# Performance work log

Hardware: AMD Instinct MI355X
Metric: run time of the kernel (lower is better)

The kernel has to match this reference:

```python
import jax, jax.numpy as jnp
import numpy as np

T = 4194304  # sequence length (2**22)

def setup_inputs() -> dict:
    key = jax.random.key(0)
    k = jax.random.split(key, 7)
    return {
        "x_0": jax.random.normal(k[0], (1, 2), dtype=jnp.float32),
        "u": jax.random.normal(k[1], (2, T), dtype=jnp.float32),
        "timedelta": jax.random.uniform(k[2], (T,), dtype=jnp.float32),
        # scale W_A down so the linear recurrence x_t = A x_{t-1} + ... is stable over 4M steps
        "W_A": 0.3 * jax.random.normal(k[3], (2, 2), dtype=jnp.float32),
        "b_A": 0.1 * jax.random.normal(k[4], (2,), dtype=jnp.float32),
        "W_B": jax.random.normal(k[5], (2, 2), dtype=jnp.float32),
        "b_B": 0.1 * jax.random.normal(k[6], (2,), dtype=jnp.float32),
    }

def reference(x_0, u, timedelta, W_A, b_A, W_B, b_B):
    # forward_PINN: linear state recurrence x_t = A x_{t-1} + B u_t (+biases),
    # output_t = physics_prediction(x_{t-1}, u_t, dt_t) - x_t
    x0 = x_0[0]          # [2] state (x, y)
    u_seq = u.T          # [T, 2] controls (speed, heading)

    def step(x_prev, inp):
        u_t, dt = inp                                  # [2], scalar
        x_t = W_A @ x_prev + b_A + W_B @ u_t + b_B     # [2]
        c = u_t[0] * dt
        pinn = x_prev + jnp.stack([c * jnp.cos(u_t[1]), c * jnp.sin(u_t[1])])
        return x_t, pinn - x_t

    _, x_out = jax.lax.scan(step, x0, (u_seq, timedelta))  # [T, 2]
    return x_out
```

## Files before the change

kernel.cpp:

```cpp
#include <hip/hip_runtime.h>

#define T_TOTAL 4194304
#define S 16
#define NTHREADS 256
#define BLOCK_T (NTHREADS * S)
#define HALO_SEG 4
#define NSEG (NTHREADS + HALO_SEG)

struct M22 { float m00, m01, m10, m11; };
__device__ __forceinline__ M22 mmul(const M22& X, const M22& Y) {
    M22 r;
    r.m00 = fmaf(X.m00, Y.m00, X.m01 * Y.m10);
    r.m01 = fmaf(X.m00, Y.m01, X.m01 * Y.m11);
    r.m10 = fmaf(X.m10, Y.m00, X.m11 * Y.m10);
    r.m11 = fmaf(X.m10, Y.m01, X.m11 * Y.m11);
    return r;
}

struct alignas(16) F16 { float f[16]; };
__device__ __forceinline__ void load16(F16& d, const float* __restrict__ p) {
    const float4* q = (const float4*)p;
    float4 a0 = q[0], a1 = q[1], a2 = q[2], a3 = q[3];
    *(float4*)&d.f[0]  = a0;
    *(float4*)&d.f[4]  = a1;
    *(float4*)&d.f[8]  = a2;
    *(float4*)&d.f[12] = a3;
}

__global__ __launch_bounds__(NTHREADS, 4)
void pinn_rnn_kernel(const float* __restrict__ x0p,
                     const float* __restrict__ u,
                     const float* __restrict__ td,
                     const float* __restrict__ WA,
                     const float* __restrict__ bA,
                     const float* __restrict__ WB,
                     const float* __restrict__ bB,
                     float* __restrict__ out)
{
    __shared__ float2 lc[NSEG];
    __shared__ float2 lout[BLOCK_T];

    const int tid = threadIdx.x;
    const int B0  = blockIdx.x * BLOCK_T;

    const float a00 = WA[0], a01 = WA[1], a10 = WA[2], a11 = WA[3];
    const float w00 = WB[0], w01 = WB[1], w10 = WB[2], w11 = WB[3];
    const float bc0 = bA[0] + bB[0];
    const float bc1 = bA[1] + bB[1];

    const float* u0 = u;
    const float* u1 = u + T_TOTAL;

    const int t0 = B0 + tid * S;
    F16 U0, U1, DT;
    load16(U0, u0 + t0);
    load16(U1, u1 + t0);
    load16(DT, td + t0);

    M22 A   = { a00, a01, a10, a11 };
    M22 A2  = mmul(A,  A );
    M22 A4  = mmul(A2, A2);
    M22 A8  = mmul(A4, A4);
    M22 M   = mmul(A8, A8);
    M22 Mp2 = mmul(M,  M );
    M22 Mp3 = mmul(Mp2, M);

    {
        float x0v = 0.f, x1v = 0.f;
        #pragma unroll
        for (int j = 0; j < S; ++j) {
            float v0 = fmaf(w00, U0.f[j], fmaf(w01, U1.f[j], bc0));
            float v1 = fmaf(w10, U0.f[j], fmaf(w11, U1.f[j], bc1));
            float n0 = fmaf(a00, x0v, fmaf(a01, x1v, v0));
            float n1 = fmaf(a10, x0v, fmaf(a11, x1v, v1));
            x0v = n0; x1v = n1;
        }
        lc[tid + HALO_SEG] = make_float2(x0v, x1v);
    }
    if (tid < HALO_SEG) {
        float2 ch = make_float2(0.f, 0.f);
        if (blockIdx.x != 0) {
            const int th = B0 - HALO_SEG * S + tid * S;
            F16 H0, H1;
            load16(H0, u0 + th);
            load16(H1, u1 + th);
            float x0v = 0.f, x1v = 0.f;
            #pragma unroll
            for (int j = 0; j < S; ++j) {
                float v0 = fmaf(w00, H0.f[j], fmaf(w01, H1.f[j], bc0));
                float v1 = fmaf(w10, H0.f[j], fmaf(w11, H1.f[j], bc1));
                float n0 = fmaf(a00, x0v, fmaf(a01, x1v, v0));
                float n1 = fmaf(a10, x0v, fmaf(a11, x1v, v1));
                x0v = n0; x1v = n1;
            }
            ch = make_float2(x0v, x1v);
        }
        lc[tid] = ch;
    }
    __syncthreads();

    float2 c1 = lc[tid + 3], c2 = lc[tid + 2], c3 = lc[tid + 1], c4 = lc[tid];
    float xi0 = c1.x
              + fmaf(M.m00,   c2.x, M.m01   * c2.y)
              + fmaf(Mp2.m00, c3.x, Mp2.m01 * c3.y)
              + fmaf(Mp3.m00, c4.x, Mp3.m01 * c4.y);
    float xi1 = c1.y
              + fmaf(M.m10,   c2.x, M.m11   * c2.y)
              + fmaf(Mp2.m10, c3.x, Mp2.m11 * c3.y)
              + fmaf(Mp3.m10, c4.x, Mp3.m11 * c4.y);

    if (blockIdx.x == 0 && tid < HALO_SEG) {
        float X0 = x0p[0], X1 = x0p[1];
        M22 P;
        if      (tid == 0) P = { 1.f, 0.f, 0.f, 1.f };
        else if (tid == 1) P = M;
        else if (tid == 2) P = Mp2;
        else               P = Mp3;
        xi0 += fmaf(P.m00, X0, P.m01 * X1);
        xi1 += fmaf(P.m10, X0, P.m11 * X1);
    }

    {
        const int xm = tid & 14;
        float2* lrow = lout + tid * S;
        float x0v = xi0, x1v = xi1;
        #pragma unroll
        for (int j = 0; j < S; ++j) {
            float v0 = fmaf(w00, U0.f[j], fmaf(w01, U1.f[j], bc0));
            float v1 = fmaf(w10, U0.f[j], fmaf(w11, U1.f[j], bc1));
            float n0 = fmaf(a00, x0v, fmaf(a01, x1v, v0));
            float n1 = fmaf(a10, x0v, fmaf(a11, x1v, v1));
            float cc = U0.f[j] * DT.f[j];
            float sn, cs;
            __sincosf(U1.f[j], &sn, &cs);
            lrow[j ^ xm] = make_float2(fmaf(cc, cs, x0v) - n0,
                                       fmaf(cc, sn, x1v) - n1);
            x0v = n0; x1v = n1;
        }
    }
    __syncthreads();

    const float4* lo4 = (const float4*)lout;
    float4* og = (float4*)out + (B0 >> 1);
    #pragma unroll
    for (int m = 0; m < 8; ++m) {
        int f    = m * NTHREADS + tid;
        int i0   = f << 1;
        int slot = i0 ^ ((i0 >> 4) & 14);
        og[f] = lo4[slot >> 1];
    }
}

extern "C" void kernel_launch(void* const* d_in, const int* in_sizes, int n_in,
                              void* d_out, int out_size, void* d_ws, size_t ws_size,
                              hipStream_t stream) {
    const float* x0p = (const float*)d_in[0];
    const float* u   = (const float*)d_in[1];
    const float* td  = (const float*)d_in[2];
    const float* WA  = (const float*)d_in[3];
    const float* bA  = (const float*)d_in[4];
    const float* WB  = (const float*)d_in[5];
    const float* bB  = (const float*)d_in[6];
    float* outp = (float*)d_out;

    dim3 grid(T_TOTAL / BLOCK_T);
    dim3 block(NTHREADS);
    pinn_rnn_kernel<<<grid, block, 0, stream>>>(x0p, u, td, WA, bA, WB, bB, outp);
}
```

Before: 106.6 us.

## Stage input loads through swizzled shared memory for coalesced global reads

Replaces the per-thread strided 64-byte vector loads of u and timedelta with fully coalesced block-wide float4 loads into a swizzled LDS buffer, which each thread then reads back as its contiguous 16-element chunk. The same LDS buffer is reused for u, then timedelta, then the output staging, so the shared-memory footprint stays the same. The aim is better global-load coalescing. In exchange it adds several barriers and LDS round trips, and the timedelta load is deferred until after the chunk-state scan.

```diff
diff --git a/kernel.cpp b/kernel.cpp
--- a/kernel.cpp
+++ b/kernel.cpp
@@ -18,13 +18,9 @@
 }
 
 struct alignas(16) F16 { float f[16]; };
-__device__ __forceinline__ void load16(F16& d, const float* __restrict__ p) {
-    const float4* q = (const float4*)p;
-    float4 a0 = q[0], a1 = q[1], a2 = q[2], a3 = q[3];
-    *(float4*)&d.f[0]  = a0;
-    *(float4*)&d.f[4]  = a1;
-    *(float4*)&d.f[8]  = a2;
-    *(float4*)&d.f[12] = a3;
+
+__device__ __forceinline__ int swz(int t, int o) {
+    return (t << 2) | (o ^ ((t >> 1) & 3));
 }
 
 __global__ __launch_bounds__(NTHREADS, 4)
@@ -37,8 +33,8 @@
                      const float* __restrict__ bB,
                      float* __restrict__ out)
 {
+    __shared__ float4 buf[2048];
     __shared__ float2 lc[NSEG];
-    __shared__ float2 lout[BLOCK_T];
 
     const int tid = threadIdx.x;
     const int B0  = blockIdx.x * BLOCK_T;
@@ -51,11 +47,34 @@
     const float* u0 = u;
     const float* u1 = u + T_TOTAL;
 
-    const int t0 = B0 + tid * S;
-    F16 U0, U1, DT;
-    load16(U0, u0 + t0);
-    load16(U1, u1 + t0);
-    load16(DT, td + t0);
+    F16 H0, H1;
+    float X0 = 0.f, X1 = 0.f;
+    const bool halo_owner = (tid < HALO_SEG);
+    if (halo_owner) {
+        if (blockIdx.x != 0) {
+            const float4* h0 = (const float4*)(u0 + B0 - HALO_SEG * S + tid * S);
+            const float4* h1 = (const float4*)(u1 + B0 - HALO_SEG * S + tid * S);
+            #pragma unroll
+            for (int o = 0; o < 4; ++o) { *(float4*)&H0.f[o*4] = h0[o];
+                                          *(float4*)&H1.f[o*4] = h1[o]; }
+        } else {
+            X0 = x0p[0]; X1 = x0p[1];
+            #pragma unroll
+            for (int o = 0; o < 4; ++o) { *(float4*)&H0.f[o*4] = make_float4(0,0,0,0);
+                                          *(float4*)&H1.f[o*4] = make_float4(0,0,0,0); }
+        }
+    }
+
+    const float4* gu0 = (const float4*)(u0 + B0);
+    const float4* gu1 = (const float4*)(u1 + B0);
+    #pragma unroll
+    for (int m = 0; m < 4; ++m) {
+        int f = m * NTHREADS + tid;
+        int t = f >> 2, o = f & 3;
+        float4 a = gu0[f], b = gu1[f];
+        buf[swz(t, o)]        = a;
+        buf[1024 + swz(t, o)] = b;
+    }
 
     M22 A   = { a00, a01, a10, a11 };
     M22 A2  = mmul(A,  A );
@@ -65,6 +84,18 @@
     M22 Mp2 = mmul(M,  M );
     M22 Mp3 = mmul(Mp2, M);
 
+    __syncthreads();
+
+    F16 U0, U1;
+    {
+        const int s = (tid >> 1) & 3;
+        #pragma unroll
+        for (int o = 0; o < 4; ++o) {
+            *(float4*)&U0.f[o*4] = buf[(tid << 2) | (o ^ s)];
+            *(float4*)&U1.f[o*4] = buf[1024 + ((tid << 2) | (o ^ s))];
+        }
+    }
+
     {
         float x0v = 0.f, x1v = 0.f;
         #pragma unroll
@@ -77,27 +108,27 @@
         }
         lc[tid + HALO_SEG] = make_float2(x0v, x1v);
     }
-    if (tid < HALO_SEG) {
-        float2 ch = make_float2(0.f, 0.f);
-        if (blockIdx.x != 0) {
-            const int th = B0 - HALO_SEG * S + tid * S;
-            F16 H0, H1;
-            load16(H0, u0 + th);
-            load16(H1, u1 + th);
-            float x0v = 0.f, x1v = 0.f;
-            #pragma unroll
-            for (int j = 0; j < S; ++j) {
-                float v0 = fmaf(w00, H0.f[j], fmaf(w01, H1.f[j], bc0));
-                float v1 = fmaf(w10, H0.f[j], fmaf(w11, H1.f[j], bc1));
-                float n0 = fmaf(a00, x0v, fmaf(a01, x1v, v0));
-                float n1 = fmaf(a10, x0v, fmaf(a11, x1v, v1));
-                x0v = n0; x1v = n1;
-            }
-            ch = make_float2(x0v, x1v);
-        }
-        lc[tid] = ch;
-    }
-    __syncthreads();
+    if (halo_owner) {
+        float x0v = 0.f, x1v = 0.f;
+        #pragma unroll
+        for (int j = 0; j < S; ++j) {
+            float v0 = fmaf(w00, H0.f[j], fmaf(w01, H1.f[j], bc0));
+            float v1 = fmaf(w10, H0.f[j], fmaf(w11, H1.f[j], bc1));
+            float n0 = fmaf(a00, x0v, fmaf(a01, x1v, v0));
+            float n1 = fmaf(a10, x0v, fmaf(a11, x1v, v1));
+            x0v = n0; x1v = n1;
+        }
+        if (blockIdx.x == 0) { x0v = 0.f; x1v = 0.f; }
+        lc[tid] = make_float2(x0v, x1v);
+    }
+    __syncthreads();
+
+    const float4* gdt = (const float4*)(td + B0);
+    #pragma unroll
+    for (int m = 0; m < 4; ++m) {
+        int f = m * NTHREADS + tid;
+        buf[swz(f >> 2, f & 3)] = gdt[f];
+    }
 
     float2 c1 = lc[tid + 3], c2 = lc[tid + 2], c3 = lc[tid + 1], c4 = lc[tid];
     float xi0 = c1.x
@@ -109,8 +140,7 @@
               + fmaf(Mp2.m10, c3.x, Mp2.m11 * c3.y)
               + fmaf(Mp3.m10, c4.x, Mp3.m11 * c4.y);
 
-    if (blockIdx.x == 0 && tid < HALO_SEG) {
-        float X0 = x0p[0], X1 = x0p[1];
+    if (blockIdx.x == 0 && halo_owner) {
         M22 P;
         if      (tid == 0) P = { 1.f, 0.f, 0.f, 1.f };
         else if (tid == 1) P = M;
@@ -119,8 +149,19 @@
         xi0 += fmaf(P.m00, X0, P.m01 * X1);
         xi1 += fmaf(P.m10, X0, P.m11 * X1);
     }
-
-    {
+    __syncthreads();
+
+    F16 DT;
+    {
+        const int s = (tid >> 1) & 3;
+        #pragma unroll
+        for (int o = 0; o < 4; ++o)
+            *(float4*)&DT.f[o*4] = buf[(tid << 2) | (o ^ s)];
+    }
+    __syncthreads();
+
+    {
+        float2* lout = (float2*)buf;
         const int xm = tid & 14;
         float2* lrow = lout + tid * S;
         float x0v = xi0, x1v = xi1;
@@ -140,7 +181,7 @@
     }
     __syncthreads();
 
-    const float4* lo4 = (const float4*)lout;
+    const float4* lo4 = (const float4*)buf;
     float4* og = (float4*)out + (B0 >> 1);
     #pragma unroll
     for (int m = 0; m < 8; ++m) {
```

Measured after the change: 105.9 us. No clear change (-0.7%).

## Process two consecutive tiles per block, reusing the first tile's chunk states as halo

Applied to the files above, without the earlier changes.

Each block now handles two back-to-back 4096-step tiles instead of one, halving the grid. The second tile's halo chunk states are copied from the first tile's shared-memory results instead of being recomputed from global memory, and the second tile's inputs are loaded early so the loads overlap the first tile's work. In exchange, each block uses double the shared memory, the occupancy hint drops from 4 to 2, and each thread holds more registers.

```diff
diff --git a/kernel.cpp b/kernel.cpp
--- a/kernel.cpp
+++ b/kernel.cpp
@@ -4,6 +4,7 @@
 #define S 16
 #define NTHREADS 256
 #define BLOCK_T (NTHREADS * S)
+#define WPB 2
 #define HALO_SEG 4
 #define NSEG (NTHREADS + HALO_SEG)
 
@@ -27,7 +28,7 @@
     *(float4*)&d.f[12] = a3;
 }
 
-__global__ __launch_bounds__(NTHREADS, 4)
+__global__ __launch_bounds__(NTHREADS, 2)
 void pinn_rnn_kernel(const float* __restrict__ x0p,
                      const float* __restrict__ u,
                      const float* __restrict__ td,
@@ -37,11 +38,12 @@
                      const float* __restrict__ bB,
                      float* __restrict__ out)
 {
-    __shared__ float2 lc[NSEG];
-    __shared__ float2 lout[BLOCK_T];
+    __shared__ float2 lc0[NSEG], lc1[NSEG];
+    __shared__ float2 lout0[BLOCK_T], lout1[BLOCK_T];
 
     const int tid = threadIdx.x;
-    const int B0  = blockIdx.x * BLOCK_T;
+    const int B0  = blockIdx.x * (WPB * BLOCK_T);
+    const int B1  = B0 + BLOCK_T;
 
     const float a00 = WA[0], a01 = WA[1], a10 = WA[2], a11 = WA[3];
     const float w00 = WB[0], w01 = WB[1], w10 = WB[2], w11 = WB[3];
@@ -52,10 +54,26 @@
     const float* u1 = u + T_TOTAL;
 
     const int t0 = B0 + tid * S;
-    F16 U0, U1, DT;
-    load16(U0, u0 + t0);
-    load16(U1, u1 + t0);
-    load16(DT, td + t0);
+    F16 U0a, U1a, DTa;
+    load16(U0a, u0 + t0);
+    load16(U1a, u1 + t0);
+    load16(DTa, td + t0);
+
+    F16 H0, H1;
+    float X0 = 0.f, X1 = 0.f;
+    const bool halo_owner = (tid < HALO_SEG);
+    if (halo_owner) {
+        if (blockIdx.x != 0) {
+            const int th = B0 - HALO_SEG * S + tid * S;
+            load16(H0, u0 + th);
+            load16(H1, u1 + th);
+        } else {
+            X0 = x0p[0]; X1 = x0p[1];
+            #pragma unroll
+            for (int o = 0; o < 4; ++o) { *(float4*)&H0.f[o*4] = make_float4(0,0,0,0);
+                                          *(float4*)&H1.f[o*4] = make_float4(0,0,0,0); }
+        }
+    }
 
     M22 A   = { a00, a01, a10, a11 };
     M22 A2  = mmul(A,  A );
@@ -69,70 +87,69 @@
         float x0v = 0.f, x1v = 0.f;
         #pragma unroll
         for (int j = 0; j < S; ++j) {
-            float v0 = fmaf(w00, U0.f[j], fmaf(w01, U1.f[j], bc0));
-            float v1 = fmaf(w10, U0.f[j], fmaf(w11, U1.f[j], bc1));
-            float n0 = fmaf(a00, x0v, fmaf(a01, x1v, v0));
-            float n1 = fmaf(a10, x0v, fmaf(a11, x1v, v1));
-            x0v = n0; x1v = n1;
-        }
-        lc[tid + HALO_SEG] = make_float2(x0v, x1v);
-    }
-    if (tid < HALO_SEG) {
-        float2 ch = make_float2(0.f, 0.f);
-        if (blockIdx.x != 0) {
-            const int th = B0 - HALO_SEG * S + tid * S;
-            F16 H0, H1;
-            load16(H0, u0 + th);
-            load16(H1, u1 + th);
-            float x0v = 0.f, x1v = 0.f;
-            #pragma unroll
-            for (int j = 0; j < S; ++j) {
-                float v0 = fmaf(w00, H0.f[j], fmaf(w01, H1.f[j], bc0));
-                float v1 = fmaf(w10, H0.f[j], fmaf(w11, H1.f[j], bc1));
-                float n0 = fmaf(a00, x0v, fmaf(a01, x1v, v0));
-                float n1 = fmaf(a10, x0v, fmaf(a11, x1v, v1));
-                x0v = n0; x1v = n1;
-            }
-            ch = make_float2(x0v, x1v);
-        }
-        lc[tid] = ch;
-    }
-    __syncthreads();
-
-    float2 c1 = lc[tid + 3], c2 = lc[tid + 2], c3 = lc[tid + 1], c4 = lc[tid];
-    float xi0 = c1.x
-              + fmaf(M.m00,   c2.x, M.m01   * c2.y)
-              + fmaf(Mp2.m00, c3.x, Mp2.m01 * c3.y)
-              + fmaf(Mp3.m00, c4.x, Mp3.m01 * c4.y);
-    float xi1 = c1.y
-              + fmaf(M.m10,   c2.x, M.m11   * c2.y)
-              + fmaf(Mp2.m10, c3.x, Mp2.m11 * c3.y)
-              + fmaf(Mp3.m10, c4.x, Mp3.m11 * c4.y);
-
-    if (blockIdx.x == 0 && tid < HALO_SEG) {
-        float X0 = x0p[0], X1 = x0p[1];
-        M22 P;
-        if      (tid == 0) P = { 1.f, 0.f, 0.f, 1.f };
-        else if (tid == 1) P = M;
-        else if (tid == 2) P = Mp2;
-        else               P = Mp3;
-        xi0 += fmaf(P.m00, X0, P.m01 * X1);
-        xi1 += fmaf(P.m10, X0, P.m11 * X1);
-    }
-
-    {
+            float v0 = fmaf(w00, U0a.f[j], fmaf(w01, U1a.f[j], bc0));
+            float v1 = fmaf(w10, U0a.f[j], fmaf(w11, U1a.f[j], bc1));
+            float n0 = fmaf(a00, x0v, fmaf(a01, x1v, v0));
+            float n1 = fmaf(a10, x0v, fmaf(a11, x1v, v1));
+            x0v = n0; x1v = n1;
+        }
+        lc0[tid + HALO_SEG] = make_float2(x0v, x1v);
+    }
+    if (halo_owner) {
+        float x0v = 0.f, x1v = 0.f;
+        #pragma unroll
+        for (int j = 0; j < S; ++j) {
+            float v0 = fmaf(w00, H0.f[j], fmaf(w01, H1.f[j], bc0));
+            float v1 = fmaf(w10, H0.f[j], fmaf(w11, H1.f[j], bc1));
+            float n0 = fmaf(a00, x0v, fmaf(a01, x1v, v0));
+            float n1 = fmaf(a10, x0v, fmaf(a11, x1v, v1));
+            x0v = n0; x1v = n1;
+        }
+        lc0[tid] = make_float2(x0v, x1v);
+        if (blockIdx.x == 0) lc0[tid] = make_float2(0.f, 0.f);
+    }
+
+    const int t1 = B1 + tid * S;
+    F16 U0b, U1b, DTb;
+    load16(U0b, u0 + t1);
+    load16(U1b, u1 + t1);
+    load16(DTb, td + t1);
+
+    __syncthreads();
+
+    if (halo_owner) lc1[tid] = lc0[NTHREADS + tid];
+
+    {
+        float2 c1 = lc0[tid + 3], c2 = lc0[tid + 2], c3 = lc0[tid + 1], c4 = lc0[tid];
+        float xi0 = c1.x
+                  + fmaf(M.m00,   c2.x, M.m01   * c2.y)
+                  + fmaf(Mp2.m00, c3.x, Mp2.m01 * c3.y)
+                  + fmaf(Mp3.m00, c4.x, Mp3.m01 * c4.y);
+        float xi1 = c1.y
+                  + fmaf(M.m10,   c2.x, M.m11   * c2.y)
+                  + fmaf(Mp2.m10, c3.x, Mp2.m11 * c3.y)
+                  + fmaf(Mp3.m10, c4.x, Mp3.m11 * c4.y);
+        if (blockIdx.x == 0 && halo_owner) {
+            M22 P;
+            if      (tid == 0) P = { 1.f, 0.f, 0.f, 1.f };
+            else if (tid == 1) P = M;
+            else if (tid == 2) P = Mp2;
+            else               P = Mp3;
+            xi0 += fmaf(P.m00, X0, P.m01 * X1);
+            xi1 += fmaf(P.m10, X0, P.m11 * X1);
+        }
         const int xm = tid & 14;
-        float2* lrow = lout + tid * S;
+        float2* lrow = lout0 + tid * S;
         float x0v = xi0, x1v = xi1;
         #pragma unroll
         for (int j = 0; j < S; ++j) {
-            float v0 = fmaf(w00, U0.f[j], fmaf(w01, U1.f[j], bc0));
-            float v1 = fmaf(w10, U0.f[j], fmaf(w11, U1.f[j], bc1));
-            float n0 = fmaf(a00, x0v, fmaf(a01, x1v, v0));
-            float n1 = fmaf(a10, x0v, fmaf(a11, x1v, v1));
-            float cc = U0.f[j] * DT.f[j];
+            float v0 = fmaf(w00, U0a.f[j], fmaf(w01, U1a.f[j], bc0));
+            float v1 = fmaf(w10, U0a.f[j], fmaf(w11, U1a.f[j], bc1));
+            float n0 = fmaf(a00, x0v, fmaf(a01, x1v, v0));
+            float n1 = fmaf(a10, x0v, fmaf(a11, x1v, v1));
+            float cc = U0a.f[j] * DTa.f[j];
             float sn, cs;
-            __sincosf(U1.f[j], &sn, &cs);
+            __sincosf(U1a.f[j], &sn, &cs);
             lrow[j ^ xm] = make_float2(fmaf(cc, cs, x0v) - n0,
                                        fmaf(cc, sn, x1v) - n1);
             x0v = n0; x1v = n1;
@@ -140,14 +157,70 @@
     }
     __syncthreads();
 
-    const float4* lo4 = (const float4*)lout;
-    float4* og = (float4*)out + (B0 >> 1);
-    #pragma unroll
-    for (int m = 0; m < 8; ++m) {
-        int f    = m * NTHREADS + tid;
-        int i0   = f << 1;
-        int slot = i0 ^ ((i0 >> 4) & 14);
-        og[f] = lo4[slot >> 1];
+    {
+        const float4* lo4 = (const float4*)lout0;
+        float4* og = (float4*)out + (B0 >> 1);
+        #pragma unroll
+        for (int m = 0; m < 8; ++m) {
+            int f    = m * NTHREADS + tid;
+            int i0   = f << 1;
+            int slot = i0 ^ ((i0 >> 4) & 14);
+            og[f] = lo4[slot >> 1];
+        }
+    }
+    {
+        float x0v = 0.f, x1v = 0.f;
+        #pragma unroll
+        for (int j = 0; j < S; ++j) {
+            float v0 = fmaf(w00, U0b.f[j], fmaf(w01, U1b.f[j], bc0));
+            float v1 = fmaf(w10, U0b.f[j], fmaf(w11, U1b.f[j], bc1));
+            float n0 = fmaf(a00, x0v, fmaf(a01, x1v, v0));
+            float n1 = fmaf(a10, x0v, fmaf(a11, x1v, v1));
+            x0v = n0; x1v = n1;
+        }
+        lc1[tid + HALO_SEG] = make_float2(x0v, x1v);
+    }
+    __syncthreads();
+
+    {
+        float2 c1 = lc1[tid + 3], c2 = lc1[tid + 2], c3 = lc1[tid + 1], c4 = lc1[tid];
+        float xi0 = c1.x
+                  + fmaf(M.m00,   c2.x, M.m01   * c2.y)
+                  + fmaf(Mp2.m00, c3.x, Mp2.m01 * c3.y)
+                  + fmaf(Mp3.m00, c4.x, Mp3.m01 * c4.y);
+        float xi1 = c1.y
+                  + fmaf(M.m10,   c2.x, M.m11   * c2.y)
+                  + fmaf(Mp2.m10, c3.x, Mp2.m11 * c3.y)
+                  + fmaf(Mp3.m10, c4.x, Mp3.m11 * c4.y);
+        const int xm = tid & 14;
+        float2* lrow = lout1 + tid * S;
+        float x0v = xi0, x1v = xi1;
+        #pragma unroll
+        for (int j = 0; j < S; ++j) {
+            float v0 = fmaf(w00, U0b.f[j], fmaf(w01, U1b.f[j], bc0));
+            float v1 = fmaf(w10, U0b.f[j], fmaf(w11, U1b.f[j], bc1));
+            float n0 = fmaf(a00, x0v, fmaf(a01, x1v, v0));
+            float n1 = fmaf(a10, x0v, fmaf(a11, x1v, v1));
+            float cc = U0b.f[j] * DTb.f[j];
+            float sn, cs;
+            __sincosf(U1b.f[j], &sn, &cs);
+            lrow[j ^ xm] = make_float2(fmaf(cc, cs, x0v) - n0,
+                                       fmaf(cc, sn, x1v) - n1);
+            x0v = n0; x1v = n1;
+        }
+    }
+    __syncthreads();
+
+    {
+        const float4* lo4 = (const float4*)lout1;
+        float4* og = (float4*)out + (B1 >> 1);
+        #pragma unroll
+        for (int m = 0; m < 8; ++m) {
+            int f    = m * NTHREADS + tid;
+            int i0   = f << 1;
+            int slot = i0 ^ ((i0 >> 4) & 14);
+            og[f] = lo4[slot >> 1];
+        }
     }
 }
 
@@ -163,7 +236,7 @@
     const float* bB  = (const float*)d_in[6];
     float* outp = (float*)d_out;
 
-    dim3 grid(T_TOTAL / BLOCK_T);
+    dim3 grid(T_TOTAL / (WPB * BLOCK_T));
     dim3 block(NTHREADS);
     pinn_rnn_kernel<<<grid, block, 0, stream>>>(x0p, u, td, WA, bA, WB, bB, outp);
 }
```

Measured after the change: 104.9 us, median of 2. No clear change (-1.6%).

## Restructure scan to wave-local windows with shuffle prefix and direct stores

Applied to the files above, without the earlier changes.

Each wavefront now processes two consecutive 1024-step windows. The carry-in is built with cross-lane shuffles instead of shared memory and barriers, and the second window is seeded by the first window's final state, which halves the halo recomputation per element. Outputs go straight to global memory as float4 stores, replacing the LDS transpose staging. The second window's loads are issued before the halo work to overlap latency. In exchange, each lane's float4 stores are strided rather than fully coalesced, register pressure is higher, and the occupancy hint is dropped.

```diff
diff --git a/kernel.cpp b/kernel.cpp
--- a/kernel.cpp
+++ b/kernel.cpp
@@ -2,10 +2,12 @@
 
 #define T_TOTAL 4194304
 #define S 16
+#define WIN 1024
+#define NWIN 2
+#define WAVE_T (WIN * NWIN)
 #define NTHREADS 256
-#define BLOCK_T (NTHREADS * S)
-#define HALO_SEG 4
-#define NSEG (NTHREADS + HALO_SEG)
+#define WAVES_PB (NTHREADS / 64)
+#define BLOCK_T (WAVE_T * WAVES_PB)
 
 struct M22 { float m00, m01, m10, m11; };
 __device__ __forceinline__ M22 mmul(const M22& X, const M22& Y) {
@@ -27,7 +29,7 @@
     *(float4*)&d.f[12] = a3;
 }
 
-__global__ __launch_bounds__(NTHREADS, 4)
+__global__ __launch_bounds__(NTHREADS)
 void pinn_rnn_kernel(const float* __restrict__ x0p,
                      const float* __restrict__ u,
                      const float* __restrict__ td,
@@ -37,118 +39,145 @@
                      const float* __restrict__ bB,
                      float* __restrict__ out)
 {
-    __shared__ float2 lc[NSEG];
-    __shared__ float2 lout[BLOCK_T];
-
-    const int tid = threadIdx.x;
-    const int B0  = blockIdx.x * BLOCK_T;
+    const int lane = threadIdx.x & 63;
+    const int gw   = blockIdx.x * WAVES_PB + (threadIdx.x >> 6);
+    const int b0   = gw * WAVE_T;
+    const int b1   = b0 + WIN;
+    const bool first = (gw == 0);
 
     const float a00 = WA[0], a01 = WA[1], a10 = WA[2], a11 = WA[3];
     const float w00 = WB[0], w01 = WB[1], w10 = WB[2], w11 = WB[3];
     const float bc0 = bA[0] + bB[0];
     const float bc1 = bA[1] + bB[1];
+    const float X0 = x0p[0], X1 = x0p[1];
 
     const float* u0 = u;
     const float* u1 = u + T_TOTAL;
 
-    const int t0 = B0 + tid * S;
-    F16 U0, U1, DT;
-    load16(U0, u0 + t0);
-    load16(U1, u1 + t0);
-    load16(DT, td + t0);
+    const int t0 = b0 + lane * S;
+    F16 U0a, U1a, DTa;
+    load16(U0a, u0 + t0);
+    load16(U1a, u1 + t0);
+    load16(DTa, td + t0);
+
+    F16 H0 = {}, H1 = {};
+    if (lane < 4 && !first) {
+        const int th = b0 - 64 + lane * S;
+        load16(H0, u0 + th);
+        load16(H1, u1 + th);
+    }
 
     M22 A   = { a00, a01, a10, a11 };
     M22 A2  = mmul(A,  A );
     M22 A4  = mmul(A2, A2);
     M22 A8  = mmul(A4, A4);
     M22 M   = mmul(A8, A8);
-    M22 Mp2 = mmul(M,  M );
-    M22 Mp3 = mmul(Mp2, M);
+    M22 M2_ = mmul(M,  M );
+    M22 M3_ = mmul(M2_, M);
 
-    {
+    auto zsr = [&](const F16& P0, const F16& P1, float& cx, float& cy) {
         float x0v = 0.f, x1v = 0.f;
         #pragma unroll
         for (int j = 0; j < S; ++j) {
-            float v0 = fmaf(w00, U0.f[j], fmaf(w01, U1.f[j], bc0));
-            float v1 = fmaf(w10, U0.f[j], fmaf(w11, U1.f[j], bc1));
+            float v0 = fmaf(w00, P0.f[j], fmaf(w01, P1.f[j], bc0));
+            float v1 = fmaf(w10, P0.f[j], fmaf(w11, P1.f[j], bc1));
             float n0 = fmaf(a00, x0v, fmaf(a01, x1v, v0));
             float n1 = fmaf(a10, x0v, fmaf(a11, x1v, v1));
             x0v = n0; x1v = n1;
         }
-        lc[tid + HALO_SEG] = make_float2(x0v, x1v);
-    }
-    if (tid < HALO_SEG) {
-        float2 ch = make_float2(0.f, 0.f);
-        if (blockIdx.x != 0) {
-            const int th = B0 - HALO_SEG * S + tid * S;
-            F16 H0, H1;
-            load16(H0, u0 + th);
-            load16(H1, u1 + th);
-            float x0v = 0.f, x1v = 0.f;
+        cx = x0v; cy = x1v;
+    };
+
+    auto prefix = [&](float cx, float cy, float xw0, float xw1,
+                      float& xi0, float& xi1) {
+        float s0 = 0.f, s1 = 0.f, tx, ty;
+        tx = __shfl_up(cx, 1); ty = __shfl_up(cy, 1);
+        if (lane >= 1) { s0 += tx; s1 += ty; }
+        tx = __shfl_up(cx, 2); ty = __shfl_up(cy, 2);
+        if (lane >= 2) { s0 += fmaf(M.m00, tx, M.m01 * ty);
+                         s1 += fmaf(M.m10, tx, M.m11 * ty); }
+        tx = __shfl_up(cx, 3); ty = __shfl_up(cy, 3);
+        if (lane >= 3) { s0 += fmaf(M2_.m00, tx, M2_.m01 * ty);
+                         s1 += fmaf(M2_.m10, tx, M2_.m11 * ty); }
+        tx = __shfl_up(cx, 4); ty = __shfl_up(cy, 4);
+        if (lane >= 4) { s0 += fmaf(M3_.m00, tx, M3_.m01 * ty);
+                         s1 += fmaf(M3_.m10, tx, M3_.m11 * ty); }
+        if (lane < 4) {
+            M22 P;
+            if      (lane == 0) P = { 1.f, 0.f, 0.f, 1.f };
+            else if (lane == 1) P = M;
+            else if (lane == 2) P = M2_;
+            else                P = M3_;
+            s0 += fmaf(P.m00, xw0, P.m01 * xw1);
+            s1 += fmaf(P.m10, xw0, P.m11 * xw1);
+        }
+        xi0 = s0; xi1 = s1;
+    };
+
+    auto replay = [&](const F16& P0, const F16& P1, const F16& PD,
+                      float xi0, float xi1, int base,
+                      float& xo0, float& xo1) {
+        float x0v = xi0, x1v = xi1;
+        float4* og = (float4*)out + (base >> 1) + lane * (S / 2);
+        #pragma unroll
+        for (int p = 0; p < S / 2; ++p) {
+            float o[4];
             #pragma unroll
-            for (int j = 0; j < S; ++j) {
-                float v0 = fmaf(w00, H0.f[j], fmaf(w01, H1.f[j], bc0));
-                float v1 = fmaf(w10, H0.f[j], fmaf(w11, H1.f[j], bc1));
+            for (int q = 0; q < 2; ++q) {
+                int j = 2 * p + q;
+                float v0 = fmaf(w00, P0.f[j], fmaf(w01, P1.f[j], bc0));
+                float v1 = fmaf(w10, P0.f[j], fmaf(w11, P1.f[j], bc1));
                 float n0 = fmaf(a00, x0v, fmaf(a01, x1v, v0));
                 float n1 = fmaf(a10, x0v, fmaf(a11, x1v, v1));
+                float cc = P0.f[j] * PD.f[j];
+                float sn, cs;
+                __sincosf(P1.f[j], &sn, &cs);
+                o[2 * q]     = fmaf(cc, cs, x0v) - n0;
+                o[2 * q + 1] = fmaf(cc, sn, x1v) - n1;
                 x0v = n0; x1v = n1;
             }
-            ch = make_float2(x0v, x1v);
+            og[p] = make_float4(o[0], o[1], o[2], o[3]);
         }
-        lc[tid] = ch;
-    }
-    __syncthreads();
+        xo0 = x0v; xo1 = x1v;
+    };
 
-    float2 c1 = lc[tid + 3], c2 = lc[tid + 2], c3 = lc[tid + 1], c4 = lc[tid];
-    float xi0 = c1.x
-              + fmaf(M.m00,   c2.x, M.m01   * c2.y)
-              + fmaf(Mp2.m00, c3.x, Mp2.m01 * c3.y)
-              + fmaf(Mp3.m00, c4.x, Mp3.m01 * c4.y);
-    float xi1 = c1.y
-              + fmaf(M.m10,   c2.x, M.m11   * c2.y)
-              + fmaf(Mp2.m10, c3.x, Mp2.m11 * c3.y)
-              + fmaf(Mp3.m10, c4.x, Mp3.m11 * c4.y);
+    float cx, cy;
+    zsr(U0a, U1a, cx, cy);
 
-    if (blockIdx.x == 0 && tid < HALO_SEG) {
-        float X0 = x0p[0], X1 = x0p[1];
-        M22 P;
-        if      (tid == 0) P = { 1.f, 0.f, 0.f, 1.f };
-        else if (tid == 1) P = M;
-        else if (tid == 2) P = Mp2;
-        else               P = Mp3;
-        xi0 += fmaf(P.m00, X0, P.m01 * X1);
-        xi1 += fmaf(P.m10, X0, P.m11 * X1);
+    const int t1 = b1 + lane * S;
+    F16 U0b, U1b, DTb;
+    load16(U0b, u0 + t1);
+    load16(U1b, u1 + t1);
+    load16(DTb, td + t1);
+
+    float xw0, xw1;
+    if (first) {
+        xw0 = X0; xw1 = X1;
+    } else {
+        float hcx, hcy;
+        zsr(H0, H1, hcx, hcy);
+        float h0x = __shfl(hcx, 0), h0y = __shfl(hcy, 0);
+        float h1x = __shfl(hcx, 1), h1y = __shfl(hcy, 1);
+        float h2x = __shfl(hcx, 2), h2y = __shfl(hcy, 2);
+        float h3x = __shfl(hcx, 3), h3y = __shfl(hcy, 3);
+        xw0 = h3x + fmaf(M.m00, h2x, M.m01 * h2y)
+                  + fmaf(M2_.m00, h1x, M2_.m01 * h1y)
+                  + fmaf(M3_.m00, h0x, M3_.m01 * h0y);
+        xw1 = h3y + fmaf(M.m10, h2x, M.m11 * h2y)
+                  + fmaf(M2_.m10, h1x, M2_.m11 * h1y)
+                  + fmaf(M3_.m10, h0x, M3_.m11 * h0y);
     }
 
-    {
-        const int xm = tid & 14;
-        float2* lrow = lout + tid * S;
-        float x0v = xi0, x1v = xi1;
-        #pragma unroll
-        for (int j = 0; j < S; ++j) {
-            float v0 = fmaf(w00, U0.f[j], fmaf(w01, U1.f[j], bc0));
-            float v1 = fmaf(w10, U0.f[j], fmaf(w11, U1.f[j], bc1));
-            float n0 = fmaf(a00, x0v, fmaf(a01, x1v, v0));
-            float n1 = fmaf(a10, x0v, fmaf(a11, x1v, v1));
-            float cc = U0.f[j] * DT.f[j];
-            float sn, cs;
-            __sincosf(U1.f[j], &sn, &cs);
-            lrow[j ^ xm] = make_float2(fmaf(cc, cs, x0v) - n0,
-                                       fmaf(cc, sn, x1v) - n1);
-            x0v = n0; x1v = n1;
-        }
-    }
-    __syncthreads();
+    float xi0, xi1, xf0, xf1;
+    prefix(cx, cy, xw0, xw1, xi0, xi1);
+    replay(U0a, U1a, DTa, xi0, xi1, b0, xf0, xf1);
 
-    const float4* lo4 = (const float4*)lout;
-    float4* og = (float4*)out + (B0 >> 1);
-    #pragma unroll
-    for (int m = 0; m < 8; ++m) {
-        int f    = m * NTHREADS + tid;
-        int i0   = f << 1;
-        int slot = i0 ^ ((i0 >> 4) & 14);
-        og[f] = lo4[slot >> 1];
-    }
+    float cw0 = __shfl(xf0, 63);
+    float cw1 = __shfl(xf1, 63);
+
+    zsr(U0b, U1b, cx, cy);
+    prefix(cx, cy, cw0, cw1, xi0, xi1);
+    replay(U0b, U1b, DTb, xi0, xi1, b1, xf0, xf1);
 }
 
 extern "C" void kernel_launch(void* const* d_in, const int* in_sizes, int n_in,
```

Result: slower. 115.2 us (+8.0%).
